# Kernel tuning notes

Measured on AMD Instinct MI355X. Metric: run time of the kernel, lower is better.

## Reference

```python
import jax, jax.numpy as jnp
from jax import lax
import numpy as np

B, T, Hh, Ww, I, D, L, N = 32, 12, 64, 128, 8, 512, 6, 16
V = I + 1          # auto + I covariates
HSZ = V            # min(D, I+1) hidden size of flattened GRN


def layer_norm(x, s, b, eps=1e-5):
    mu = jnp.mean(x, -1, keepdims=True)
    var = jnp.mean((x - mu) ** 2, -1, keepdims=True)
    return (x - mu) / jnp.sqrt(var + eps) * s + b


def interp1d(x, out_size):
    # F.interpolate(mode='linear', align_corners=True) over last axis
    n = x.shape[-1]
    pos = jnp.arange(out_size, dtype=x.dtype) * ((n - 1) / (out_size - 1))
    lo = jnp.floor(pos).astype(jnp.int32)
    hi = jnp.minimum(lo + 1, n - 1)
    frac = pos - lo.astype(x.dtype)
    return x[..., lo] * (1.0 - frac) + x[..., hi] * frac


def pconv(x, m, w, b, stride):
    # NVIDIA-style partial conv, single-channel mask, VALID padding
    kh, kw = w.shape[-2], w.shape[-1]
    dn = ('NCHW', 'OIHW', 'NCHW')
    summ = lax.conv_general_dilated(m, jnp.ones((1, 1, kh, kw), x.dtype), stride, 'VALID', dimension_numbers=dn)
    ratio = (kh * kw) / (summ + 1e-8)
    upd = jnp.clip(summ, 0.0, 1.0)
    ratio = ratio * upd
    raw = lax.conv_general_dilated(x * m, w, stride, 'VALID', dimension_numbers=dn)
    return (raw * ratio + b[None, :, None, None]) * upd, upd


def lstm_last(x, wih, whh, bih, bhh):
    # torch nn.LSTM (1 layer, batch_first), zero init state; return last hidden
    d = whh.shape[1]
    def step(carry, xt):
        h, c = carry
        g = xt @ wih.T + bih + h @ whh.T + bhh
        i, f, gg, o = jnp.split(g, 4, -1)
        c = jax.nn.sigmoid(f) * c + jax.nn.sigmoid(i) * jnp.tanh(gg)
        h = jax.nn.sigmoid(o) * jnp.tanh(c)
        return (h, c), None
    z = jnp.zeros((x.shape[0], d), x.dtype)
    (h, _), _ = lax.scan(step, (z, z), jnp.swapaxes(x, 0, 1))
    return h


def varsel(xin, rn_gate, rn_scale, rn_bias, fc1_w, fc1_b, fc2_w, fc2_b,
           glu_w, glu_b, grn_ln_s, grn_ln_b, rs_gate, rs_scale, rs_bias):
    # pytorch_forecasting VariableSelectionNetwork, all inputs pre-embedded (flag=True)
    # xin: [..., V, D]
    v = layer_norm(xin * (2.0 * jax.nn.sigmoid(rn_gate)), rn_scale, rn_bias)  # per-var ResampleNorm
    flat = xin.reshape(xin.shape[:-2] + (V * D,))
    # flattened GRN (residual=False): residual = ResampleNorm(flat -> V)
    res = layer_norm(interp1d(flat, V) * (2.0 * jax.nn.sigmoid(rs_gate)), rs_scale, rs_bias)
    h = jax.nn.elu(flat @ fc1_w.T + fc1_b)
    h = h @ fc2_w.T + fc2_b
    g = h @ glu_w.T + glu_b
    a, gb = jnp.split(g, 2, -1)
    wgt = jax.nn.softmax(layer_norm(a * jax.nn.sigmoid(gb) + res, grn_ln_s, grn_ln_b), -1)  # [..., V]
    return jnp.einsum('...vd,...v->...d', v, wgt), wgt


def reference(Xauto, Xcov, Xstatic, xmask,
              conv1_w, conv1_b, conv2_w, conv2_b, conv3_w, conv3_b,
              cov_w, static_w,
              rn_gate, rn_scale, rn_bias,
              fc1_w, fc1_b, fc2_w, fc2_b, glu_w, glu_b, grn_ln_s, grn_ln_b,
              rs_gate, rs_scale, rs_bias,
              ln1_s, ln1_b, ln2_s, ln2_b, ln3_s, ln3_b,
              lstm_wih, lstm_whh, lstm_bih, lstm_bhh,
              head_w, head_b):
    vsn = (rn_gate, rn_scale, rn_bias, fc1_w, fc1_b, fc2_w, fc2_b,
           glu_w, glu_b, grn_ln_s, grn_ln_b, rs_gate, rs_scale, rs_bias)
    # static embedding for shifts -T+1..L  -> [B, T+L, D]
    Xs = jnp.stack([jnp.roll(Xstatic, s, axis=1) for s in range(-T + 1, L + 1)], 1)
    Xs = Xs @ static_w.T
    Xs_lag, Xs_lead = Xs[:, :T], Xs[:, T:]
    # partial-conv auto embedding, all timesteps folded into batch
    m0 = xmask[0:1]
    x = Xauto.reshape(B * T, 1, Hh, Ww)
    h1, m1 = pconv(x, m0, conv1_w, conv1_b, (2, 2))
    h2, m2 = pconv(h1, m1, conv2_w, conv2_b, (2, 2))
    h3, _ = pconv(h2, m2, conv3_w, conv3_b, (Hh // 4, Ww // 4))  # [B*T, D, 1, 1]
    Xauto_emb = h3.reshape(B, T, D)
    Xcov_emb = jnp.einsum('bti,id->btid', Xcov, cov_w)           # Linear(1,D) per covariate
    Xemb = jnp.concatenate([Xauto_emb[:, :, None], Xcov_emb], 2)  # [B,T,V,D]
    Xsel, w_all = varsel(Xemb + Xs_lag[:, :, None], *vsn)        # [B,T,D], [B,T,V]
    wgts = [w_all[:, -1]]
    Xcur = layer_norm(Xsel, ln1_s, ln1_b)                        # [B,T,D]
    cov_last = Xcov_emb[:, -1]                                   # [B,I,D]
    yemb = []
    for l in range(L):
        h = lstm_last(Xcur, lstm_wih, lstm_whh, lstm_bih, lstm_bhh)
        ydec = layer_norm(h, ln2_s, ln2_b) + Xs_lead[:, l]
        yemb.append(ydec)
        if l < L - 1:
            xin2 = jnp.concatenate([ydec[:, None], cov_last], 1) + Xs_lead[:, l][:, None]
            xout, w = varsel(xin2, *vsn)
            wgts.append(w)
            Xcur = layer_norm(xout, ln3_s, ln3_b)[:, None]
    yemb = jnp.stack(yemb, 1)                                    # [B,L,D]
    Y = (yemb @ head_w.T + head_b).reshape(B, L, N, Hh, Ww)
    return Y, jnp.stack(wgts, 1)


def setup_inputs():
    key = jax.random.key(0)
    ks = jax.random.split(key, 16)
    f32 = jnp.float32
    def nrm(k, shape): return jax.random.normal(k, shape, f32) * 0.02
    return dict(
        Xauto=jax.random.normal(ks[0], (B, T, Hh, Ww), f32),
        Xcov=jax.random.normal(ks[1], (B, T, I), f32),
        Xstatic=jax.random.normal(ks[2], (B, 12), f32),
        xmask=jax.random.uniform(ks[3], (B, 1, Hh, Ww), dtype=f32),
        conv1_w=nrm(ks[4], (D // 4, 1, 2, 2)), conv1_b=jnp.zeros((D // 4,), f32),
        conv2_w=nrm(ks[5], (D // 2, D // 4, 2, 2)), conv2_b=jnp.zeros((D // 2,), f32),
        conv3_w=nrm(ks[6], (D, D // 2, Hh // 4, Ww // 4)), conv3_b=jnp.zeros((D,), f32),
        cov_w=nrm(ks[7], (I, D)),
        static_w=nrm(ks[8], (D, 12)),
        rn_gate=jnp.zeros((V, D), f32), rn_scale=jnp.ones((V, D), f32), rn_bias=jnp.zeros((V, D), f32),
        fc1_w=nrm(ks[9], (HSZ, V * D)), fc1_b=jnp.zeros((HSZ,), f32),
        fc2_w=nrm(ks[10], (HSZ, HSZ)), fc2_b=jnp.zeros((HSZ,), f32),
        glu_w=nrm(ks[11], (2 * V, HSZ)), glu_b=jnp.zeros((2 * V,), f32),
        grn_ln_s=jnp.ones((V,), f32), grn_ln_b=jnp.zeros((V,), f32),
        rs_gate=jnp.zeros((V,), f32), rs_scale=jnp.ones((V,), f32), rs_bias=jnp.zeros((V,), f32),
        ln1_s=jnp.ones((D,), f32), ln1_b=jnp.zeros((D,), f32),
        ln2_s=jnp.ones((D,), f32), ln2_b=jnp.zeros((D,), f32),
        ln3_s=jnp.ones((D,), f32), ln3_b=jnp.zeros((D,), f32),
        lstm_wih=nrm(ks[12], (4 * D, D)), lstm_whh=nrm(ks[13], (4 * D, D)),
        lstm_bih=jnp.zeros((4 * D,), f32), lstm_bhh=jnp.zeros((4 * D,), f32),
        head_w=nrm(ks[14], (N * Hh * Ww, D)), head_b=jnp.zeros((N * Hh * Ww,), f32),
    )
```

## Files before the change

### kernel.cpp

```cpp
#include <hip/hip_runtime.h>
#include <hip/hip_bf16.h>

#define DEV __device__ __forceinline__

namespace {
constexpr size_t WS_XS   = 8192;
constexpr size_t WS_H3   = WS_XS + 294912;
constexpr size_t WS_XCUR = WS_H3 + 196608;
constexpr size_t WS_XPROJ= WS_XCUR + 196608;
constexpr size_t WS_HB0  = WS_XPROJ + 786432;
constexpr size_t WS_HB1  = WS_HB0 + 16384;
constexpr size_t WS_CB   = WS_HB1 + 16384;
constexpr size_t WS_YDEC = WS_CB + 16384;
constexpr size_t WS_YEMBB= WS_YDEC + 16384;
constexpr size_t WS_GB   = WS_YEMBB + 49152;
constexpr size_t WS_XC1  = WS_GB + 65536;
constexpr size_t WS_W12  = WS_XC1 + 16384;
constexpr size_t WS_ENDF = WS_W12 + 8192;
constexpr size_t A2_BYTES = 100663296ull;
constexpr int YN = 25165824;
}

typedef __bf16 b16x8 __attribute__((ext_vector_type(8)));
typedef float  f32x4 __attribute__((ext_vector_type(4)));

DEV float sigm(float x){ return 1.f/(1.f+expf(-x)); }

DEV unsigned short f2b(float x){ __hip_bfloat16 h=__float2bfloat16(x); return *reinterpret_cast<unsigned short*>(&h); }

DEV void gload16(const unsigned short* g, unsigned short* l){
  __builtin_amdgcn_global_load_lds((const __attribute__((address_space(1))) void*)g,
                                   (__attribute__((address_space(3))) void*)l, 16, 0, 0);
}

DEV float blockReduceSum256(float v, float* red){
  const int tid = threadIdx.x;
  red[tid]=v; __syncthreads();
  #pragma unroll
  for(int s=128;s>0;s>>=1){ if(tid<s) red[tid]+=red[tid+s]; __syncthreads(); }
  const float r = red[0]; __syncthreads();
  return r;
}

DEV float2 blockReduceSum2(float a, float b, float* red){
  #pragma unroll
  for(int off=32; off>0; off>>=1){
    a += __shfl_xor(a, off);
    b += __shfl_xor(b, off);
  }
  const int wid = threadIdx.x>>6;
  __syncthreads();
  if((threadIdx.x&63)==0){ red[wid*2]=a; red[wid*2+1]=b; }
  __syncthreads();
  float2 r;
  r.x = red[0]+red[2]+red[4]+red[6];
  r.y = red[1]+red[3]+red[5]+red[7];
  return r;
}

__global__ __launch_bounds__(256) void k_pre(const float* __restrict__ xmask,
                                             const float* __restrict__ c1w, const float* __restrict__ c1b,
                                             const float* __restrict__ c2w,
                                             const float* __restrict__ rn_gate,
                                             const float* __restrict__ bih, const float* __restrict__ bhh,
                                             const float* __restrict__ Xstat, const float* __restrict__ static_w,
                                             float* __restrict__ ws,
                                             float* __restrict__ W12, float* __restrict__ WB,
                                             float* __restrict__ g2, float* __restrict__ bsum,
                                             float* __restrict__ XS){
  const int tid=threadIdx.x;
  if(blockIdx.x==0){
    float* R1  = ws;
    float* U1S = ws+2048;
    float* R2  = ws+4096;
    float* U2S = ws+4608;
    float* SC  = ws+5120;
    float* RU  = ws+5632;
    __shared__ float u1[2048];
    __shared__ float u2[512];
    __shared__ float red[256];
    for(int idx=tid; idx<2048; idx+=256){
      const int y=idx>>6, x=idx&63;
      const float s = xmask[(2*y)*128+2*x]+xmask[(2*y)*128+2*x+1]
                    + xmask[(2*y+1)*128+2*x]+xmask[(2*y+1)*128+2*x+1];
      const float u = fminf(fmaxf(s,0.f),1.f);
      const float r = 4.f/(s+1e-8f)*u;
      R1[idx]=r; U1S[idx]=u*u; RU[idx]=r*u*u; u1[idx]=u;
    }
    __syncthreads();
    for(int idx=tid; idx<512; idx+=256){
      const int y=idx>>5, x=idx&31;
      const float s = u1[(2*y)*64+2*x]+u1[(2*y)*64+2*x+1]+u1[(2*y+1)*64+2*x]+u1[(2*y+1)*64+2*x+1];
      const float u=fminf(fmaxf(s,0.f),1.f);
      R2[idx]=4.f/(s+1e-8f)*u; U2S[idx]=u*u; u2[idx]=u;
    }
    __syncthreads();
    float p=0; for(int idx=tid; idx<512; idx+=256) p+=u2[idx];
    const float s3 = blockReduceSum256(p,red);
    if(tid==0){ const float u=fminf(fmaxf(s3,0.f),1.f); SC[0]=512.f/(s3+1e-8f)*u; SC[1]=u; }
  } else if(blockIdx.x==1){
    const int oc=tid;
    for(int i=oc;i<4608;i+=256) g2[i]=2.f*sigm(rn_gate[i]);
    for(int i=oc;i<2048;i+=256) bsum[i]=bih[i]+bhh[i];
    float acc[16]={}; float accb[4]={};
    for(int ic=0;ic<128;ic++){
      const float4 w2=*(const float4*)&c2w[oc*512+ic*4];
      const float4 w1=*(const float4*)&c1w[ic*4];
      const float b1=c1b[ic];
      const float w2a[4]={w2.x,w2.y,w2.z,w2.w};
      const float w1a[4]={w1.x,w1.y,w1.z,w1.w};
      #pragma unroll
      for(int dydx=0;dydx<4;dydx++){
        const int dy=dydx>>1, dx=dydx&1;
        #pragma unroll
        for(int uv=0;uv<4;uv++){
          const int u=uv>>1, v=uv&1;
          acc[(2*dy+u)*4 + (2*dx+v)] = fmaf(w2a[dydx], w1a[uv], acc[(2*dy+u)*4+(2*dx+v)]);
        }
        accb[dydx] = fmaf(w2a[dydx], b1, accb[dydx]);
      }
    }
    #pragma unroll
    for(int t=0;t<16;t++) W12[oc*16+t]=acc[t];
    #pragma unroll
    for(int t=0;t<4;t++) WB[oc*4+t]=accb[t];
  } else {
    const int gid=(blockIdx.x-2)*256+tid;
    if(gid < 32*18*512){
      const int d = gid&511, row = gid>>9;
      const int b = row/18, si = row - b*18;
      const int s = si-11;
      float acc=0.f;
      #pragma unroll
      for(int j=0;j<12;j++){
        int idx = j - s; idx %= 12; if(idx<0) idx+=12;
        acc = fmaf(Xstat[b*12+idx], static_w[d*12+j], acc);
      }
      XS[gid]=acc;
    }
  }
}

__global__ __launch_bounds__(256) void k_conv12(const float* __restrict__ Xauto, const float* __restrict__ xmask,
                                                const float* __restrict__ wsm,
                                                const float* __restrict__ W12, const float* __restrict__ WB,
                                                const float* __restrict__ c2b,
                                                unsigned short* __restrict__ A2){
  const int img=blockIdx.x, tid=threadIdx.x;
  __shared__ float S[64][132];
  __shared__ float u1s[2048];
  __shared__ float w12[4096];
  __shared__ float wb4[1024];
  __shared__ float r2s[512], u2s[512], cb[256];
  for(int i=tid;i<8192;i+=256){
    const int Y=i>>7, X=i&127;
    S[Y][X] = Xauto[(size_t)img*8192 + i] * xmask[i] * wsm[5632 + (Y>>1)*64 + (X>>1)];
  }
  for(int i=tid;i<2048;i+=256) u1s[i]=wsm[2048+i];
  for(int i=tid;i<4096;i+=256) w12[i]=W12[i];
  for(int i=tid;i<1024;i+=256) wb4[i]=WB[i];
  for(int i=tid;i<512;i+=256){ r2s[i]=wsm[4096+i]; u2s[i]=wsm[4608+i]; }
  if(tid<256) cb[tid]=c2b[tid];
  __syncthreads();
  float s16[2][16], us4[2][4], r2[2], u2[2];
  #pragma unroll
  for(int half=0;half<2;half++){
    const int p=tid+half*256;
    const int y2=p>>5, x2=p&31;
    #pragma unroll
    for(int ty=0;ty<4;ty++){
      const float4 v=*(const float4*)&S[4*y2+ty][4*x2];
      s16[half][ty*4+0]=v.x; s16[half][ty*4+1]=v.y; s16[half][ty*4+2]=v.z; s16[half][ty*4+3]=v.w;
    }
    #pragma unroll
    for(int dd=0;dd<4;dd++)
      us4[half][dd]=u1s[(2*y2+(dd>>1))*64 + (2*x2+(dd&1))];
    r2[half]=r2s[p]; u2[half]=u2s[p];
  }
  for(int oc=0;oc<256;oc++){
    const float4 w0=*(const float4*)&w12[oc*16];
    const float4 w1=*(const float4*)&w12[oc*16+4];
    const float4 w2=*(const float4*)&w12[oc*16+8];
    const float4 w3=*(const float4*)&w12[oc*16+12];
    const float4 wb=*(const float4*)&wb4[oc*4];
    const float cbo=cb[oc];
    #pragma unroll
    for(int half=0;half<2;half++){
      const float* s=s16[half];
      float a =  w0.x*s[0]+w0.y*s[1]+w0.z*s[2]+w0.w*s[3];
      a = fmaf(w1.x,s[4],fmaf(w1.y,s[5],fmaf(w1.z,s[6],fmaf(w1.w,s[7],a))));
      a = fmaf(w2.x,s[8],fmaf(w2.y,s[9],fmaf(w2.z,s[10],fmaf(w2.w,s[11],a))));
      a = fmaf(w3.x,s[12],fmaf(w3.y,s[13],fmaf(w3.z,s[14],fmaf(w3.w,s[15],a))));
      a += wb.x*us4[half][0]+wb.y*us4[half][1]+wb.z*us4[half][2]+wb.w*us4[half][3];
      const float v=(a*r2[half]+cbo)*u2[half];
      A2[(size_t)img*131072 + oc*512 + tid + half*256] = f2b(v);
    }
  }
}

template<int MODE, int BM, int BN, int NT>
__global__ __launch_bounds__(NT) void k_mfma(const unsigned short* __restrict__ Aq,
                                             const float* __restrict__ Bq,
                                             float* __restrict__ Cp,
                                             const float* __restrict__ bias0){
  constexpr int BK=64, CH=8;
  constexpr bool AF32 = (MODE==3);
  constexpr int NWN=2, NWM=(NT/64)/NWN;
  constexpr int RW=BM/NWM, CW=BN/NWN;
  constexpr int FM=RW/16, FN=CW/16;
  constexpr int NA=BM*CH/NT, NB=BN*CH/NT;
  constexpr int ABYTES=2*BM*BK*2, BBYTES=2*BN*BK*2;
  constexpr int CP=BN+4;
  constexpr int CSB=RW*CP*4;
  constexpr int SMB=(ABYTES+BBYTES>CSB)?(ABYTES+BBYTES):CSB;
  __shared__ __align__(16) char smem[SMB];
  unsigned short* lA=(unsigned short*)smem;
  unsigned short* lB=(unsigned short*)(smem+ABYTES);
  const int tid=threadIdx.x, lane=tid&63;
  const int w=tid>>6, wn=w&1, wm=w>>1;
  const int m0=blockIdx.y*BM, n0=blockIdx.x*BN;
  constexpr size_t lda=(MODE==1)?131072:512;
  constexpr size_t ldb=(MODE==1)?131072:512;
  int kbeg=0, kend=512;
  if constexpr(MODE==1){ kbeg=blockIdx.z*2048; kend=kbeg+2048; }

  f32x4 acc[FM][FN];
  #pragma unroll
  for(int i=0;i<FM;i++)
    #pragma unroll
    for(int j=0;j<FN;j++) acc[i][j]=f32x4{0.f,0.f,0.f,0.f};

  float4 bufB[NB][2];
  float4 bufA[AF32?NA:1][2];
  auto stageA=[&](int k0, int buf){
    #pragma unroll
    for(int i=0;i<NA;i++){
      const int c=tid+i*NT, r=c>>3, gk=c&7;
      gload16(Aq + (size_t)(m0+r)*lda + k0 + ((gk ^ (r&7))<<3),
              lA + (size_t)buf*BM*64 + c*8);
    }
  };
  auto fetchA=[&](int k0){
    if constexpr(AF32){
      #pragma unroll
      for(int i=0;i<NA;i++){
        const int c=tid+i*NT, r=c>>3, gk=c&7;
        const float* p=(const float*)Aq + (size_t)(m0+r)*lda + k0+gk*8;
        bufA[i][0]=*(const float4*)p; bufA[i][1]=*(const float4*)(p+4);
      }
    }
  };
  auto commitA=[&](int buf){
    if constexpr(AF32){
      #pragma unroll
      for(int i=0;i<NA;i++){
        const int c=tid+i*NT, r=c>>3, gk=c&7;
        union { unsigned short us[8]; int4 q; } u;
        const float4 a=bufA[i][0], b=bufA[i][1];
        u.us[0]=f2b(a.x); u.us[1]=f2b(a.y); u.us[2]=f2b(a.z); u.us[3]=f2b(a.w);
        u.us[4]=f2b(b.x); u.us[5]=f2b(b.y); u.us[6]=f2b(b.z); u.us[7]=f2b(b.w);
        *(int4*)(lA + (size_t)buf*BM*64 + ((size_t)r*8 + (gk ^ (r&7)))*8)=u.q;
      }
    }
  };
  auto fetchB=[&](int k0){
    #pragma unroll
    for(int i=0;i<NB;i++){
      const int c=tid+i*NT, r=c>>3, gk=c&7;
      const float* p=Bq + (size_t)(n0+r)*ldb + k0+gk*8;
      bufB[i][0]=*(const float4*)p; bufB[i][1]=*(const float4*)(p+4);
    }
  };
  auto commitB=[&](int buf){
    #pragma unroll
    for(int i=0;i<NB;i++){
      const int c=tid+i*NT, r=c>>3, gk=c&7;
      union { unsigned short us[8]; int4 q; } u;
      const float4 a=bufB[i][0], b=bufB[i][1];
      u.us[0]=f2b(a.x); u.us[1]=f2b(a.y); u.us[2]=f2b(a.z); u.us[3]=f2b(a.w);
      u.us[4]=f2b(b.x); u.us[5]=f2b(b.y); u.us[6]=f2b(b.z); u.us[7]=f2b(b.w);
      *(int4*)(lB + (size_t)buf*BN*64 + ((size_t)gk*BN + r)*8)=u.q;
    }
  };

  int cur=0;
  if constexpr(AF32) fetchA(kbeg); else stageA(kbeg,0);
  fetchB(kbeg);
  if constexpr(AF32) commitA(0);
  commitB(0);
  __syncthreads();
  for(int k0=kbeg; k0<kend; k0+=BK){
    const bool nxt=(k0+BK<kend);
    if(nxt){
      if constexpr(AF32) fetchA(k0+BK); else stageA(k0+BK, cur^1);
      fetchB(k0+BK);
    }
    #pragma unroll
    for(int ks=0; ks<2; ks++){
      const int gkr=ks*4+(lane>>4);
      b16x8 av[FM], bv[FN];
      #pragma unroll
      for(int i=0;i<FM;i++){
        const int row=wm*RW+i*16+(lane&15);
        av[i]=*(const b16x8*)(lA + (size_t)cur*BM*64 + row*64 + ((gkr ^ (row&7))<<3));
      }
      #pragma unroll
      for(int j=0;j<FN;j++){
        const int row=wn*CW+j*16+(lane&15);
        bv[j]=*(const b16x8*)(lB + (size_t)cur*BN*64 + ((size_t)gkr*BN + row)*8);
      }
      #pragma unroll
      for(int i=0;i<FM;i++)
        #pragma unroll
        for(int j=0;j<FN;j++)
          acc[i][j]=__builtin_amdgcn_mfma_f32_16x16x32_bf16(av[i],bv[j],acc[i][j],0,0,0);
    }
    if(nxt){
      if constexpr(AF32) commitA(cur^1);
      commitB(cur^1);
    }
    __syncthreads();
    cur^=1;
  }

  const int r4=(lane>>4)*4, cl=lane&15;
  float (*cs)[CP]=(float(*)[CP])smem;
  for(int ch=0; ch<NWM; ++ch){
    __syncthreads();
    if(wm==ch){
      #pragma unroll
      for(int i=0;i<FM;i++)
        #pragma unroll
        for(int j=0;j<FN;j++)
          #pragma unroll
          for(int ri=0;ri<4;ri++)
            cs[i*16+r4+ri][wn*CW+j*16+cl]=acc[i][j][ri];
    }
    __syncthreads();
    for(int idx=tid; idx<RW*(BN/4); idx+=NT){
      const int row=idx/(BN/4), q=idx%(BN/4);
      float4 v=*(float4*)&cs[row][q*4];
      const int gr=m0+ch*RW+row;
      if constexpr(MODE==1){
        *(float4*)&Cp[((size_t)blockIdx.z*384+gr)*512 + n0+q*4]=v;
      } else if constexpr(MODE==3){
        const float4 b=*(const float4*)&bias0[n0+q*4];
        v.x+=b.x; v.y+=b.y; v.z+=b.z; v.w+=b.w;
        *(float4*)&Cp[(size_t)gr*2048 + n0+q*4]=v;
      } else {
        const float4 b=*(const float4*)&bias0[n0+q*4];
        v.x+=b.x; v.y+=b.y; v.z+=b.z; v.w+=b.w;
        *(float4*)&Cp[(size_t)gr*131072 + n0+q*4]=v;
      }
    }
  }
}

__global__ __launch_bounds__(256) void k_varsel(
  const float* __restrict__ part, const float* __restrict__ c3b, const float* __restrict__ wsm,
  const float* __restrict__ Xcov, const float* __restrict__ cov_w,
  const float* __restrict__ Xs, const float* __restrict__ g2,
  const float* __restrict__ rn_scale, const float* __restrict__ rn_bias,
  const float* __restrict__ fc1_w, const float* __restrict__ fc1_b,
  const float* __restrict__ fc2_w, const float* __restrict__ fc2_b,
  const float* __restrict__ glu_w, const float* __restrict__ glu_b,
  const float* __restrict__ grn_s, const float* __restrict__ grn_b,
  const float* __restrict__ rs_gate, const float* __restrict__ rs_scale, const float* __restrict__ rs_bias,
  const float* __restrict__ lns, const float* __restrict__ lnb,
  float* __restrict__ outX, float* __restrict__ wgt_base)
{
  __shared__ float xin[9][512];
  __shared__ float red[256];
  __shared__ float obuf[512];
  __shared__ float muv[9], rsv[9], wsmx[9], hbuf9[9];
  const int tid=threadIdx.x, tk=blockIdx.x;
  const int b=tk/12, t=tk-b*12;
  const float* xs=Xs+((size_t)b*18+t)*512;
  const float* covrow=Xcov+(size_t)tk*8;
  float* orow=outX+(size_t)tk*512;
  float* wp=(t==11)? wgt_base+b*54 : nullptr;
  for(int idx=512+tid; idx<4608; idx+=256){
    const int vv=idx>>9, d=idx&511;
    xin[vv][d] = fmaf(covrow[vv-1], cov_w[(vv-1)*512+d], xs[d]);
  }
  {
    const float r3=wsm[5120], u3=wsm[5121];
    const int d0=tid*2;
    float2 s={0.f,0.f};
    const float* pr=part + (size_t)tk*512 + d0;
    #pragma unroll 4
    for(int z=0;z<64;z++){
      const float2 v=*(const float2*)(pr + (size_t)z*196608);
      s.x+=v.x; s.y+=v.y;
    }
    xin[0][d0]  =(s.x*r3+c3b[d0])  *u3 + xs[d0];
    xin[0][d0+1]=(s.y*r3+c3b[d0+1])*u3 + xs[d0+1];
  }
  __syncthreads();
  {
    float sa9[9], sb9[9];
    const int d0=tid*2;
    #pragma unroll
    for(int vv=0;vv<9;vv++){
      const float y0=xin[vv][d0]  *g2[vv*512+d0];
      const float y1=xin[vv][d0+1]*g2[vv*512+d0+1];
      sa9[vv]=y0+y1; sb9[vv]=y0*y0+y1*y1;
    }
    #pragma unroll
    for(int off=32; off>0; off>>=1){
      #pragma unroll
      for(int vv=0;vv<9;vv++){
        sa9[vv]+=__shfl_xor(sa9[vv],off);
        sb9[vv]+=__shfl_xor(sb9[vv],off);
      }
    }
    const int wid=tid>>6;
    if((tid&63)==0){
      #pragma unroll
      for(int vv=0;vv<9;vv++){ red[wid*18+vv]=sa9[vv]; red[wid*18+9+vv]=sb9[vv]; }
    }
    __syncthreads();
    if(tid<9){
      const float sA=red[tid]+red[18+tid]+red[36+tid]+red[54+tid];
      const float sB=red[9+tid]+red[27+tid]+red[45+tid]+red[63+tid];
      const float mu=sA*(1.f/512.f);
      const float var=sB*(1.f/512.f)-mu*mu;
      muv[tid]=mu; rsv[tid]=rsqrtf(var+1e-5f);
    }
  }
  {
    float hp[9]={0,0,0,0,0,0,0,0,0};
    const float* flat=&xin[0][0];
    for(int i=tid;i<4608;i+=256){
      const float f=flat[i];
      #pragma unroll
      for(int j=0;j<9;j++) hp[j]=fmaf(f, fc1_w[j*4608+i], hp[j]);
    }
    #pragma unroll
    for(int off=32; off>0; off>>=1){
      #pragma unroll
      for(int j=0;j<9;j++) hp[j]+=__shfl_xor(hp[j],off);
    }
    const int wid=tid>>6;
    __syncthreads();
    if((tid&63)==0){
      #pragma unroll
      for(int j=0;j<9;j++) red[wid*9+j]=hp[j];
    }
    __syncthreads();
    if(tid<9) hbuf9[tid]=red[tid]+red[9+tid]+red[18+tid]+red[27+tid];
    __syncthreads();
  }
  if(tid==0){
    const float* flat=&xin[0][0];
    float rg[9];
    #pragma unroll
    for(int k=0;k<9;k++){
      const float pos=(float)k*575.875f;
      const int lo=(int)floorf(pos);
      const float fr=pos-(float)lo;
      int hi=lo+1; if(hi>4607)hi=4607;
      rg[k]=(flat[lo]*(1.f-fr)+flat[hi]*fr)*2.f*sigm(rs_gate[k]);
    }
    float mu=0.f; for(int k=0;k<9;k++) mu+=rg[k]; mu*=(1.f/9.f);
    float va=0.f; for(int k=0;k<9;k++){const float dd=rg[k]-mu; va+=dd*dd;} va*=(1.f/9.f);
    float rstd=rsqrtf(va+1e-5f);
    float resv[9];
    for(int k=0;k<9;k++) resv[k]=(rg[k]-mu)*rstd*rs_scale[k]+rs_bias[k];
    float h[9];
    for(int j=0;j<9;j++){ const float x=hbuf9[j]+fc1_b[j]; h[j]=x>0.f?x:expm1f(x); }
    float h2[9];
    for(int j=0;j<9;j++){ float s=fc2_b[j]; for(int k=0;k<9;k++) s=fmaf(h[k],fc2_w[j*9+k],s); h2[j]=s; }
    float lg[9];
    for(int j=0;j<9;j++){
      float sa=glu_b[j];   for(int k=0;k<9;k++) sa=fmaf(h2[k],glu_w[j*9+k],sa);
      float sg=glu_b[9+j]; for(int k=0;k<9;k++) sg=fmaf(h2[k],glu_w[(9+j)*9+k],sg);
      lg[j]=sa*sigm(sg)+resv[j];
    }
    mu=0.f; for(int k=0;k<9;k++) mu+=lg[k]; mu*=(1.f/9.f);
    va=0.f; for(int k=0;k<9;k++){const float dd=lg[k]-mu; va+=dd*dd;} va*=(1.f/9.f);
    rstd=rsqrtf(va+1e-5f);
    float lnv[9], mx=-1e30f;
    for(int k=0;k<9;k++){ lnv[k]=(lg[k]-mu)*rstd*grn_s[k]+grn_b[k]; mx=fmaxf(mx,lnv[k]); }
    float se=0.f;
    for(int k=0;k<9;k++){ lnv[k]=expf(lnv[k]-mx); se+=lnv[k]; }
    const float inv=1.f/se;
    for(int k=0;k<9;k++){ const float w=lnv[k]*inv; wsmx[k]=w; if(wp) wp[k]=w; }
  }
  __syncthreads();
  for(int d=tid; d<512; d+=256){
    float o=0.f;
    #pragma unroll
    for(int vv=0;vv<9;vv++){
      const float y=xin[vv][d]*g2[vv*512+d];
      const float vval=(y-muv[vv])*rsv[vv]*rn_scale[vv*512+d]+rn_bias[vv*512+d];
      o=fmaf(vval,wsmx[vv],o);
    }
    obuf[d]=o;
  }
  __syncthreads();
  float sa=0.f, sb=0.f;
  for(int d=tid;d<512;d+=256){ const float v=obuf[d]; sa+=v; sb+=v*v; }
  const float2 s2=blockReduceSum2(sa, sb, red);
  const float mu2=s2.x*(1.f/512.f);
  const float var2=s2.y*(1.f/512.f)-mu2*mu2;
  const float rstd2=rsqrtf(var2+1e-5f);
  for(int d=tid;d<512;d+=256) orow[d]=(obuf[d]-mu2)*rstd2*lns[d]+lnb[d];
}

__global__ __launch_bounds__(256) void k_lstm_s(const float* __restrict__ xproj, const float* __restrict__ whh,
     const float* __restrict__ hr, float* __restrict__ hw, float* __restrict__ cg, int t){
  __shared__ float wlds[8][516];
  __shared__ float hlds[32][516];
  __shared__ float gv[32][9];
  const int bid=blockIdx.x, tid=threadIdx.x;
  const int j0=bid*2;
  for(int idx=tid; idx<1024; idx+=256){
    const int r2=idx>>7, k4=(idx&127)*4;
    const int gate2=r2>>1, jl2=r2&1;
    *(float4*)&wlds[r2][k4] = *(const float4*)&whh[(size_t)(gate2*512 + j0 + jl2)*512 + k4];
  }
  if(t>0){
    for(int idx=tid; idx<4096; idx+=256){
      const int rb=idx>>7, k4=(idx&127)*4;
      *(float4*)&hlds[rb][k4] = *(const float4*)&hr[rb*512+k4];
    }
  }
  __syncthreads();
  const int r=tid&7, b=tid>>3;
  const int gate=r>>1, jloc=r&1;
  float acc = xproj[((size_t)b*12+t)*2048 + gate*512 + j0 + jloc];
  if(t>0){
    float4 s={0.f,0.f,0.f,0.f};
    for(int k=0;k<512;k+=4){
      const float4 hk=*(const float4*)&hlds[b][k];
      const float4 wk=*(const float4*)&wlds[r][k];
      s.x=fmaf(hk.x,wk.x,s.x); s.y=fmaf(hk.y,wk.y,s.y);
      s.z=fmaf(hk.z,wk.z,s.z); s.w=fmaf(hk.w,wk.w,s.w);
    }
    acc+=(s.x+s.y)+(s.z+s.w);
  }
  gv[b][r]=acc;
  __syncthreads();
  if(tid<64){
    const int bb=tid>>1, jj=tid&1;
    const float gi=gv[bb][0+jj], gf=gv[bb][2+jj], gg=gv[bb][4+jj], go=gv[bb][6+jj];
    float c = (t==0) ? 0.f : cg[bb*512 + j0 + jj];
    c = sigm(gf)*c + sigm(gi)*tanhf(gg);
    cg[bb*512 + j0 + jj]=c;
    hw[bb*512 + j0 + jj]=sigm(go)*tanhf(c);
  }
}

__global__ __launch_bounds__(256) void k_declstm(const float* __restrict__ Xc1, const float* __restrict__ wih,
        const float* __restrict__ bsum, float* __restrict__ hout){
  __shared__ float xs_[32][516];
  const int n=blockIdx.x, tid=threadIdx.x;
  for(int idx=tid; idx<16384; idx+=256){
    const int bb=idx>>9, k=idx&511;
    xs_[bb][k]=Xc1[bb*512+k];
  }
  __syncthreads();
  const int jl=tid>>4, bl=tid&15;
  const int j=n*16+jl;
  const float* wi=wih+(size_t)j*512;
  const float* wg=wih+(size_t)(1024+j)*512;
  const float* wo=wih+(size_t)(1536+j)*512;
  const float bi_=bsum[j];
  const float bg_=bsum[1024+j];
  const float bo_=bsum[1536+j];
  #pragma unroll
  for(int half=0; half<2; half++){
    const int b=bl+half*16;
    float gi=bi_, gg=bg_, go=bo_;
    for(int k=0;k<512;k+=4){
      const float4 xk=*(const float4*)&xs_[b][k];
      const float4 a0=*(const float4*)(wi+k);
      const float4 a1=*(const float4*)(wg+k);
      const float4 a2=*(const float4*)(wo+k);
      gi += xk.x*a0.x+xk.y*a0.y+xk.z*a0.z+xk.w*a0.w;
      gg += xk.x*a1.x+xk.y*a1.y+xk.z*a1.z+xk.w*a1.w;
      go += xk.x*a2.x+xk.y*a2.y+xk.z*a2.z+xk.w*a2.w;
    }
    const float c=sigm(gi)*tanhf(gg);
    hout[b*512+j]=sigm(go)*tanhf(c);
  }
}

__global__ __launch_bounds__(256) void k_ydvs(
  int l,
  const float* __restrict__ hb, const float* __restrict__ Xcov, const float* __restrict__ cov_w,
  const float* __restrict__ Xs, const float* __restrict__ g2,
  const float* __restrict__ rn_scale, const float* __restrict__ rn_bias,
  const float* __restrict__ fc1_w, const float* __restrict__ fc1_b,
  const float* __restrict__ fc2_w, const float* __restrict__ fc2_b,
  const float* __restrict__ glu_w, const float* __restrict__ glu_b,
  const float* __restrict__ grn_s, const float* __restrict__ grn_b,
  const float* __restrict__ rs_gate, const float* __restrict__ rs_scale, const float* __restrict__ rs_bias,
  const float* __restrict__ ln2s, const float* __restrict__ ln2b,
  const float* __restrict__ ln3s, const float* __restrict__ ln3b,
  float* __restrict__ outX, float* __restrict__ wgt_base, unsigned short* __restrict__ yembB)
{
  __shared__ float xin[9][512];
  __shared__ float red[256];
  __shared__ float obuf[512];
  __shared__ float ydl[512];
  __shared__ float muv[9], rsv[9], wsmx[9], hbuf9[9];
  const int tid=threadIdx.x, b=blockIdx.x;
  const float* xs=Xs+((size_t)b*18+12+l)*512;
  for(int d=tid;d<512;d+=256) obuf[d]=hb[b*512+d];
  __syncthreads();
  {
    float sa=0.f, sb=0.f;
    for(int d=tid;d<512;d+=256){ const float v=obuf[d]; sa+=v; sb+=v*v; }
    const float2 s2=blockReduceSum2(sa, sb, red);
    const float mu=s2.x*(1.f/512.f);
    const float var=s2.y*(1.f/512.f)-mu*mu;
    const float rstd=rsqrtf(var+1e-5f);
    for(int d=tid;d<512;d+=256){
      const float o=(obuf[d]-mu)*rstd*ln2s[d]+ln2b[d]+xs[d];
      ydl[d]=o;
      yembB[((size_t)b*6+l)*512+d]=f2b(o);
    }
  }
  __syncthreads();
  if(l==5) return;
  const float* covrow=Xcov+((size_t)b*12+11)*8;
  float* orow=outX+(size_t)b*512;
  float* wp=wgt_base+b*54+(l+1)*9;
  for(int idx=tid; idx<4608; idx+=256){
    const int vv=idx>>9, d=idx&511;
    const float base=xs[d];
    xin[vv][d] = (vv==0) ? (ydl[d]+base) : fmaf(covrow[vv-1], cov_w[(vv-1)*512+d], base);
  }
  __syncthreads();
  {
    float sa9[9], sb9[9];
    const int d0=tid*2;
    #pragma unroll
    for(int vv=0;vv<9;vv++){
      const float y0=xin[vv][d0]  *g2[vv*512+d0];
      const float y1=xin[vv][d0+1]*g2[vv*512+d0+1];
      sa9[vv]=y0+y1; sb9[vv]=y0*y0+y1*y1;
    }
    #pragma unroll
    for(int off=32; off>0; off>>=1){
      #pragma unroll
      for(int vv=0;vv<9;vv++){
        sa9[vv]+=__shfl_xor(sa9[vv],off);
        sb9[vv]+=__shfl_xor(sb9[vv],off);
      }
    }
    const int wid=tid>>6;
    if((tid&63)==0){
      #pragma unroll
      for(int vv=0;vv<9;vv++){ red[wid*18+vv]=sa9[vv]; red[wid*18+9+vv]=sb9[vv]; }
    }
    __syncthreads();
    if(tid<9){
      const float sA=red[tid]+red[18+tid]+red[36+tid]+red[54+tid];
      const float sB=red[9+tid]+red[27+tid]+red[45+tid]+red[63+tid];
      const float mu=sA*(1.f/512.f);
      const float var=sB*(1.f/512.f)-mu*mu;
      muv[tid]=mu; rsv[tid]=rsqrtf(var+1e-5f);
    }
  }
  {
    float hp[9]={0,0,0,0,0,0,0,0,0};
    const float* flat=&xin[0][0];
    for(int i=tid;i<4608;i+=256){
      const float f=flat[i];
      #pragma unroll
      for(int j=0;j<9;j++) hp[j]=fmaf(f, fc1_w[j*4608+i], hp[j]);
    }
    #pragma unroll
    for(int off=32; off>0; off>>=1){
      #pragma unroll
      for(int j=0;j<9;j++) hp[j]+=__shfl_xor(hp[j],off);
    }
    const int wid=tid>>6;
    __syncthreads();
    if((tid&63)==0){
      #pragma unroll
      for(int j=0;j<9;j++) red[wid*9+j]=hp[j];
    }
    __syncthreads();
    if(tid<9) hbuf9[tid]=red[tid]+red[9+tid]+red[18+tid]+red[27+tid];
    __syncthreads();
  }
  if(tid==0){
    const float* flat=&xin[0][0];
    float rg[9];
    #pragma unroll
    for(int k=0;k<9;k++){
      const float pos=(float)k*575.875f;
      const int lo=(int)floorf(pos);
      const float fr=pos-(float)lo;
      int hi=lo+1; if(hi>4607)hi=4607;
      rg[k]=(flat[lo]*(1.f-fr)+flat[hi]*fr)*2.f*sigm(rs_gate[k]);
    }
    float mu=0.f; for(int k=0;k<9;k++) mu+=rg[k]; mu*=(1.f/9.f);
    float va=0.f; for(int k=0;k<9;k++){const float dd=rg[k]-mu; va+=dd*dd;} va*=(1.f/9.f);
    float rstd=rsqrtf(va+1e-5f);
    float resv[9];
    for(int k=0;k<9;k++) resv[k]=(rg[k]-mu)*rstd*rs_scale[k]+rs_bias[k];
    float h[9];
    for(int j=0;j<9;j++){ const float x=hbuf9[j]+fc1_b[j]; h[j]=x>0.f?x:expm1f(x); }
    float h2[9];
    for(int j=0;j<9;j++){ float s=fc2_b[j]; for(int k=0;k<9;k++) s=fmaf(h[k],fc2_w[j*9+k],s); h2[j]=s; }
    float lg[9];
    for(int j=0;j<9;j++){
      float sa=glu_b[j];   for(int k=0;k<9;k++) sa=fmaf(h2[k],glu_w[j*9+k],sa);
      float sg=glu_b[9+j]; for(int k=0;k<9;k++) sg=fmaf(h2[k],glu_w[(9+j)*9+k],sg);
      lg[j]=sa*sigm(sg)+resv[j];
    }
    mu=0.f; for(int k=0;k<9;k++) mu+=lg[k]; mu*=(1.f/9.f);
    va=0.f; for(int k=0;k<9;k++){const float dd=lg[k]-mu; va+=dd*dd;} va*=(1.f/9.f);
    rstd=rsqrtf(va+1e-5f);
    float lnv[9], mx=-1e30f;
    for(int k=0;k<9;k++){ lnv[k]=(lg[k]-mu)*rstd*grn_s[k]+grn_b[k]; mx=fmaxf(mx,lnv[k]); }
    float se=0.f;
    for(int k=0;k<9;k++){ lnv[k]=expf(lnv[k]-mx); se+=lnv[k]; }
    const float inv=1.f/se;
    for(int k=0;k<9;k++){ const float w=lnv[k]*inv; wsmx[k]=w; wp[k]=w; }
  }
  __syncthreads();
  for(int d=tid; d<512; d+=256){
    float o=0.f;
    #pragma unroll
    for(int vv=0;vv<9;vv++){
      const float y=xin[vv][d]*g2[vv*512+d];
      const float vval=(y-muv[vv])*rsv[vv]*rn_scale[vv*512+d]+rn_bias[vv*512+d];
      o=fmaf(vval,wsmx[vv],o);
    }
    obuf[d]=o;
  }
  __syncthreads();
  float sa=0.f, sb=0.f;
  for(int d=tid;d<512;d+=256){ const float v=obuf[d]; sa+=v; sb+=v*v; }
  const float2 s2=blockReduceSum2(sa, sb, red);
  const float mu2=s2.x*(1.f/512.f);
  const float var2=s2.y*(1.f/512.f)-mu2*mu2;
  const float rstd2=rsqrtf(var2+1e-5f);
  for(int d=tid;d<512;d+=256) orow[d]=(obuf[d]-mu2)*rstd2*ln3s[d]+ln3b[d];
}

extern "C" void kernel_launch(void* const* d_in, const int* in_sizes, int n_in,
                              void* d_out, int out_size, void* d_ws, size_t ws_size,
                              hipStream_t stream){
  (void)in_sizes; (void)n_in; (void)out_size; (void)ws_size;
  const float* Xauto=(const float*)d_in[0];
  const float* Xcov =(const float*)d_in[1];
  const float* Xstat=(const float*)d_in[2];
  const float* xmask=(const float*)d_in[3];
  const float* c1w=(const float*)d_in[4];
  const float* c1b=(const float*)d_in[5];
  const float* c2w=(const float*)d_in[6];
  const float* c2b=(const float*)d_in[7];
  const float* c3w=(const float*)d_in[8];
  const float* c3b=(const float*)d_in[9];
  const float* cov_w=(const float*)d_in[10];
  const float* static_w=(const float*)d_in[11];
  const float* rn_gate=(const float*)d_in[12];
  const float* rn_scale=(const float*)d_in[13];
  const float* rn_bias=(const float*)d_in[14];
  const float* fc1_w=(const float*)d_in[15];
  const float* fc1_b=(const float*)d_in[16];
  const float* fc2_w=(const float*)d_in[17];
  const float* fc2_b=(const float*)d_in[18];
  const float* glu_w=(const float*)d_in[19];
  const float* glu_b=(const float*)d_in[20];
  const float* grn_s=(const float*)d_in[21];
  const float* grn_b=(const float*)d_in[22];
  const float* rs_gate=(const float*)d_in[23];
  const float* rs_scale=(const float*)d_in[24];
  const float* rs_bias=(const float*)d_in[25];
  const float* ln1s=(const float*)d_in[26];
  const float* ln1b=(const float*)d_in[27];
  const float* ln2s=(const float*)d_in[28];
  const float* ln2b=(const float*)d_in[29];
  const float* ln3s=(const float*)d_in[30];
  const float* ln3b=(const float*)d_in[31];
  const float* wih=(const float*)d_in[32];
  const float* whh=(const float*)d_in[33];
  const float* bih=(const float*)d_in[34];
  const float* bhh=(const float*)d_in[35];
  const float* head_w=(const float*)d_in[36];
  const float* head_b=(const float*)d_in[37];

  float* out=(float*)d_out;
  float* ws=(float*)d_ws;
  unsigned short* A2=(unsigned short*)((char*)d_ws + WS_ENDF*sizeof(float));
  float* part=(float*)((char*)d_ws + WS_ENDF*sizeof(float) + A2_BYTES);
  unsigned short* yembB=(unsigned short*)(ws+WS_YEMBB);
  float* g2=ws+WS_YDEC;
  float* bsum=ws+WS_YDEC+8192;

  const dim3 blk(256);
  k_pre<<<1154,blk,0,stream>>>(xmask, c1w, c1b, c2w, rn_gate, bih, bhh, Xstat, static_w,
                               ws, ws+WS_W12, ws+WS_W12+4096, g2, bsum, ws+WS_XS);
  k_conv12<<<384,blk,0,stream>>>(Xauto, xmask, ws, ws+WS_W12, ws+WS_W12+4096, c2b, A2);
  k_mfma<1,384,128,512><<<dim3(4,1,64),dim3(512),0,stream>>>(A2, c3w, part, nullptr);
  k_varsel<<<384,blk,0,stream>>>(part, c3b, ws, Xcov, cov_w, ws+WS_XS, g2,
      rn_scale,rn_bias, fc1_w,fc1_b,fc2_w,fc2_b, glu_w,glu_b, grn_s,grn_b,
      rs_gate,rs_scale,rs_bias, ln1s,ln1b, ws+WS_XCUR, out+YN);
  k_mfma<3,192,128,512><<<dim3(16,2),dim3(512),0,stream>>>(
      (const unsigned short*)(const void*)(ws+WS_XCUR), wih, ws+WS_XPROJ, bsum);
  for(int t=0;t<12;t++){
    const float* hr = ws + ((t&1) ? WS_HB1 : WS_HB0);
    float* hw = ws + ((t&1) ? WS_HB0 : WS_HB1);
    k_lstm_s<<<256,blk,0,stream>>>(ws+WS_XPROJ, whh, hr, hw, ws+WS_CB, t);
  }
  for(int l=0;l<6;l++){
    if(l>0){
      k_declstm<<<32,blk,0,stream>>>(ws+WS_XC1, wih, bsum, ws+WS_HB0);
    }
    k_ydvs<<<32,blk,0,stream>>>(l, ws+WS_HB0, Xcov, cov_w, ws+WS_XS, g2,
        rn_scale,rn_bias, fc1_w,fc1_b,fc2_w,fc2_b, glu_w,glu_b, grn_s,grn_b,
        rs_gate,rs_scale,rs_bias, ln2s,ln2b, ln3s,ln3b,
        ws+WS_XC1, out+YN, yembB);
  }
  k_mfma<2,192,128,512><<<dim3(1024,1),dim3(512),0,stream>>>(yembB, head_w, out, head_b);
}
```

Before: 709.3 us.

## Prefetch B tiles two stages ahead with double register buffers in GEMM

The GEMM main loop is restructured into an unrolled two-stage pipeline. B tiles are now fetched into alternating register buffers two K-steps ahead, and committed to LDS one step ahead. This gives the fp32 B global loads more latency slack before they are converted and written to shared memory. The cost is doubled register use for B staging, which can lower occupancy. The loop also assumes the K range is a multiple of 2*BK.

```diff
diff --git a/kernel.cpp b/kernel.cpp
--- a/kernel.cpp
+++ b/kernel.cpp
@@ -230,7 +230,7 @@
     #pragma unroll
     for(int j=0;j<FN;j++) acc[i][j]=f32x4{0.f,0.f,0.f,0.f};
 
-  float4 bufB[NB][2];
+  float4 bufBa[NB][2], bufBb[NB][2];
   float4 bufA[AF32?NA:1][2];
   auto stageA=[&](int k0, int buf){
     #pragma unroll
@@ -263,38 +263,26 @@
       }
     }
   };
-  auto fetchB=[&](int k0){
+  auto fetchBto=[&](float4 (&dst)[NB][2], int k0){
     #pragma unroll
     for(int i=0;i<NB;i++){
       const int c=tid+i*NT, r=c>>3, gk=c&7;
       const float* p=Bq + (size_t)(n0+r)*ldb + k0+gk*8;
-      bufB[i][0]=*(const float4*)p; bufB[i][1]=*(const float4*)(p+4);
+      dst[i][0]=*(const float4*)p; dst[i][1]=*(const float4*)(p+4);
     }
   };
-  auto commitB=[&](int buf){
+  auto commitBfrom=[&](float4 (&src)[NB][2], int buf){
     #pragma unroll
     for(int i=0;i<NB;i++){
       const int c=tid+i*NT, r=c>>3, gk=c&7;
       union { unsigned short us[8]; int4 q; } u;
-      const float4 a=bufB[i][0], b=bufB[i][1];
+      const float4 a=src[i][0], b=src[i][1];
       u.us[0]=f2b(a.x); u.us[1]=f2b(a.y); u.us[2]=f2b(a.z); u.us[3]=f2b(a.w);
       u.us[4]=f2b(b.x); u.us[5]=f2b(b.y); u.us[6]=f2b(b.z); u.us[7]=f2b(b.w);
       *(int4*)(lB + (size_t)buf*BN*64 + ((size_t)gk*BN + r)*8)=u.q;
     }
   };
-
-  int cur=0;
-  if constexpr(AF32) fetchA(kbeg); else stageA(kbeg,0);
-  fetchB(kbeg);
-  if constexpr(AF32) commitA(0);
-  commitB(0);
-  __syncthreads();
-  for(int k0=kbeg; k0<kend; k0+=BK){
-    const bool nxt=(k0+BK<kend);
-    if(nxt){
-      if constexpr(AF32) fetchA(k0+BK); else stageA(k0+BK, cur^1);
-      fetchB(k0+BK);
-    }
+  auto domfma=[&](int buf){
     #pragma unroll
     for(int ks=0; ks<2; ks++){
       const int gkr=ks*4+(lane>>4);
@@ -302,12 +290,12 @@
       #pragma unroll
       for(int i=0;i<FM;i++){
         const int row=wm*RW+i*16+(lane&15);
-        av[i]=*(const b16x8*)(lA + (size_t)cur*BM*64 + row*64 + ((gkr ^ (row&7))<<3));
+        av[i]=*(const b16x8*)(lA + (size_t)buf*BM*64 + row*64 + ((gkr ^ (row&7))<<3));
       }
       #pragma unroll
       for(int j=0;j<FN;j++){
         const int row=wn*CW+j*16+(lane&15);
-        bv[j]=*(const b16x8*)(lB + (size_t)cur*BN*64 + ((size_t)gkr*BN + row)*8);
+        bv[j]=*(const b16x8*)(lB + (size_t)buf*BN*64 + ((size_t)gkr*BN + row)*8);
       }
       #pragma unroll
       for(int i=0;i<FM;i++)
@@ -315,12 +303,34 @@
         for(int j=0;j<FN;j++)
           acc[i][j]=__builtin_amdgcn_mfma_f32_16x16x32_bf16(av[i],bv[j],acc[i][j],0,0,0);
     }
-    if(nxt){
-      if constexpr(AF32) commitA(cur^1);
-      commitB(cur^1);
-    }
-    __syncthreads();
-    cur^=1;
+  };
+
+  if constexpr(AF32) fetchA(kbeg); else stageA(kbeg,0);
+  fetchBto(bufBa, kbeg);
+  if constexpr(AF32) commitA(0);
+  commitBfrom(bufBa, 0);
+  fetchBto(bufBa, kbeg+BK);
+  __syncthreads();
+  for(int k=kbeg; k<kend; k+=2*BK){
+    {
+      if(k+2*BK<kend) fetchBto(bufBb, k+2*BK);
+      if constexpr(AF32) fetchA(k+BK); else stageA(k+BK, 1);
+      commitBfrom(bufBa, 1);
+      domfma(0);
+      if constexpr(AF32) commitA(1);
+      __syncthreads();
+    }
+    {
+      const bool n1 = (k+2*BK)<kend;
+      if(k+3*BK<kend) fetchBto(bufBa, k+3*BK);
+      if(n1){
+        if constexpr(AF32) fetchA(k+2*BK); else stageA(k+2*BK, 0);
+        commitBfrom(bufBb, 0);
+      }
+      domfma(1);
+      if(n1){ if constexpr(AF32) commitA(0); }
+      __syncthreads();
+    }
   }
 
   const int r4=(lane>>4)*4, cl=lane&15;
```

New measurement: 719.7 us. About the same (+1.5%).
